# Kernel optimization log

Measured on AMD Instinct MI355X. Metric: run time of the kernel, lower is better.

The kernel has to match this reference:

```python
import jax, jax.numpy as jnp
import numpy as np

N_NODES, N_EDGES = 50000, 800000
IN_CH, HID, HEADS, OUT_CH = 128, 64, 4, 2
NEG_SLOPE = 0.2
EPS = 1e-16


def setup_inputs() -> dict:
    key = jax.random.key(0)
    ks = jax.random.split(key, 16)
    def rn(k, shape, scale=0.1):
        return jax.random.normal(k, shape, dtype=jnp.float32) * scale
    inp = {
        "x": jax.random.normal(ks[0], (N_NODES, IN_CH), dtype=jnp.float32),
        "edge_index": jax.random.randint(ks[1], (2, N_EDGES), 0, N_NODES, dtype=jnp.int64),
        "stats": jax.random.normal(ks[2], (N_EDGES, 3), dtype=jnp.float32),
        # conv1: GATConv(IN_CH -> HID, heads=HEADS, concat=True)
        "W1": rn(ks[3], (IN_CH, HEADS * HID)),
        "att_src1": rn(ks[4], (HEADS, HID)),
        "att_dst1": rn(ks[5], (HEADS, HID)),
        "b1": rn(ks[6], (HEADS * HID,)),
        # conv2: GATConv(HEADS*HID -> HID, heads=1, concat=False)
        "W2": rn(ks[7], (HEADS * HID, HID)),
        "att_src2": rn(ks[8], (1, HID)),
        "att_dst2": rn(ks[9], (1, HID)),
        "b2": rn(ks[10], (HID,)),
        # edge MLP: Linear(2*HID+3 -> HID) -> ReLU -> Linear(HID -> OUT_CH)
        "mW1": rn(ks[11], (2 * HID + 3, HID)),
        "mb1": rn(ks[12], (HID,)),
        "mW2": rn(ks[13], (HID, OUT_CH)),
        "mb2": rn(ks[14], (OUT_CH,)),
    }
    return inp


def gat_layer(x, src, dst, W, att_s, att_d, n_nodes):
    """PyG GATConv core: per-edge attention, softmax over destination, scatter-add."""
    H, C = att_s.shape
    h = (x @ W).reshape(n_nodes, H, C)                      # [N,H,C]
    a_s = jnp.sum(h * att_s, axis=-1)                        # [N,H]
    a_d = jnp.sum(h * att_d, axis=-1)                        # [N,H]
    e = a_s[src] + a_d[dst]                                  # [E,H]
    e = jnp.where(e > 0, e, NEG_SLOPE * e)                   # leaky_relu
    m = jax.ops.segment_max(e, dst, num_segments=n_nodes)    # [N,H]
    m = jnp.where(jnp.isfinite(m), m, 0.0)
    e = jnp.exp(e - m[dst])
    s = jax.ops.segment_sum(e, dst, num_segments=n_nodes)    # [N,H]
    alpha = e / (s[dst] + EPS)                               # [E,H]
    out = jax.ops.segment_sum(alpha[:, :, None] * h[src], dst, num_segments=n_nodes)
    return out                                               # [N,H,C]


def reference(x, edge_index, stats, W1, att_src1, att_dst1, b1,
              W2, att_src2, att_dst2, b2, mW1, mb1, mW2, mb2):
    n = x.shape[0]
    row, col = edge_index[0], edge_index[1]
    # add self loops (PyG GATConv default)
    loop = jnp.arange(n, dtype=edge_index.dtype)
    src = jnp.concatenate([row, loop])
    dst = jnp.concatenate([col, loop])

    # conv1: heads concatenated, then ELU (dropout disabled at inference)
    h1 = gat_layer(x, src, dst, W1, att_src1, att_dst1, n)
    h1 = h1.reshape(n, HEADS * HID) + b1
    h1 = jax.nn.elu(h1)

    # conv2: single head, concat=False (mean over 1 head == squeeze)
    h2 = gat_layer(h1, src, dst, W2, att_src2, att_dst2, n)
    node_emb = h2[:, 0, :] + b2                              # [N,HID]

    # edge MLP over gathered endpoint embeddings + per-edge stats
    feat = jnp.concatenate([node_emb[row], node_emb[col], stats], axis=1)  # [E,2*HID+3]
    hidden = jax.nn.relu(feat @ mW1 + mb1)
    return hidden @ mW2 + mb2                                # [E,OUT_CH]
```

## Files before the change

kernel.cpp:

```cpp
#include <hip/hip_runtime.h>
#include <math.h>

#define NN 50000
#define NE 800000
#define EP (NE + NN)
#define INC 128
#define HID 64
#define HEADS 4
#define C1 (HEADS * HID)
#define NEG 0.2f
#define EPSS 1e-16f

#define SCHUNK 512
#define NSB ((NN + SCHUNK - 1) / SCHUNK)

#define KP1 136
#define KP2 264
typedef __attribute__((ext_vector_type(8))) short bf16x8;
typedef __attribute__((ext_vector_type(4))) float f32x4;

__device__ __forceinline__ unsigned short f2bf(float f) {
    unsigned u = __float_as_uint(f);
    unsigned r = (u + 0x7FFFu + ((u >> 16) & 1u)) >> 16;
    return (unsigned short)r;
}
__device__ __forceinline__ float bf2f(unsigned short b) {
    return __uint_as_float(((unsigned)b) << 16);
}

__global__ __launch_bounds__(SCHUNK) void scan_partial(const int* __restrict__ counts,
                                                       int* __restrict__ bsum) {
    __shared__ int lds[SCHUNK];
    int i = blockIdx.x * SCHUNK + threadIdx.x;
    lds[threadIdx.x] = (i < NN) ? counts[i] : 0;
    __syncthreads();
    for (int off = SCHUNK / 2; off > 0; off >>= 1) {
        if (threadIdx.x < off) lds[threadIdx.x] += lds[threadIdx.x + off];
        __syncthreads();
    }
    if (threadIdx.x == 0) bsum[blockIdx.x] = lds[0];
}

__global__ void scan_top(int* __restrict__ bsum, int* __restrict__ rowptr) {
    __shared__ int lds[NSB];
    int t = threadIdx.x;
    if (t < NSB) lds[t] = bsum[t];
    __syncthreads();
    if (t == 0) {
        int acc = 0;
        for (int i = 0; i < NSB; ++i) { int v = lds[i]; lds[i] = acc; acc += v; }
        rowptr[NN] = acc;
    }
    __syncthreads();
    if (t < NSB) bsum[t] = lds[t];
}

__global__ __launch_bounds__(SCHUNK) void scan_final(const int* __restrict__ counts,
                                                     const int* __restrict__ bsum,
                                                     int* __restrict__ rowptr,
                                                     int* __restrict__ cursor) {
    __shared__ int lds[SCHUNK];
    int i = blockIdx.x * SCHUNK + threadIdx.x;
    int v = (i < NN) ? counts[i] : 0;
    lds[threadIdx.x] = v;
    __syncthreads();
    for (int off = 1; off < SCHUNK; off <<= 1) {
        int t = (threadIdx.x >= off) ? lds[threadIdx.x - off] : 0;
        __syncthreads();
        lds[threadIdx.x] += t;
        __syncthreads();
    }
    if (i < NN) {
        int excl = lds[threadIdx.x] - v + bsum[blockIdx.x];
        rowptr[i] = excl;
        cursor[i] = excl;
    }
}

__global__ void csr_fill(const int* __restrict__ ei, int* __restrict__ cursor,
                         int* __restrict__ csr_src, int* __restrict__ csr_dst) {
    int e = blockIdx.x * 256 + threadIdx.x;
    if (e >= EP) return;
    int s, d;
    if (e < NE) { s = ei[e]; d = ei[NE + e]; } else { s = d = e - NE; }
    int pos = atomicAdd(&cursor[d], 1);
    csr_src[pos] = s;
    csr_dst[pos] = d;
}

#define PREP_N0 (C1 * INC)
#define PREP_N1 (HID * C1)
#define PREP_N2 (5 * 4 * 64 * 8)
#define PREP_TOT (PREP_N0 + PREP_N1 + PREP_N2)
__global__ void prep_all(const float* __restrict__ mW1, const float* __restrict__ W1,
                         const float* __restrict__ W2, const int* __restrict__ ei,
                         unsigned short* __restrict__ w1h, unsigned short* __restrict__ w1l,
                         unsigned short* __restrict__ w2h, unsigned short* __restrict__ w2l,
                         unsigned short* __restrict__ wFh, unsigned short* __restrict__ wFl,
                         int* __restrict__ counts) {
    int i = blockIdx.x * 256 + threadIdx.x;
    if (i < PREP_N0) {
        int c = i >> 7, k = i & 127;
        float f = W1[k * C1 + c];
        unsigned short h = f2bf(f);
        w1h[i] = h; w1l[i] = f2bf(f - bf2f(h));
        return;
    }
    i -= PREP_N0;
    if (i < PREP_N1) {
        int c = i >> 8, k = i & 255;
        float f = W2[k * HID + c];
        unsigned short h = f2bf(f);
        w2h[i] = h; w2l[i] = f2bf(f - bf2f(h));
        return;
    }
    i -= PREP_N1;
    if (i < PREP_N2) {
        int kk = i >> 11;
        int ct = (i >> 9) & 3;
        int l  = (i >> 3) & 63;
        int j  = i & 7;
        int cl = l & 15, g = l >> 4;
        int k   = kk * 32 + g * 8 + j;
        int col = ct * 16 + cl;
        unsigned short h = 0, lo = 0;
        if (k < 131) {
            float f = mW1[k * 64 + col];
            h  = f2bf(f);
            lo = f2bf(f - bf2f(h));
        }
        wFh[i] = h;
        wFl[i] = lo;
        return;
    }
    i -= PREP_N2;
    if (i < EP) {
        int d = (i < NE) ? ei[NE + i] : (i - NE);
        atomicAdd(&counts[d], 1);
    }
}

__global__ void edge_w1k(const int* __restrict__ csr_src, const int* __restrict__ csr_dst,
                         const float* __restrict__ as1, const float* __restrict__ ad1,
                         float* __restrict__ w1e) {
    int i = blockIdx.x * 256 + threadIdx.x;
    if (i >= EP) return;
    int s = csr_src[i], d = csr_dst[i];
    float4 a = *(const float4*)(as1 + s * 4);
    float4 b = *(const float4*)(ad1 + d * 4);
    float4 o;
    float t;
    t = a.x + b.x; t = t > 0.f ? t : NEG * t; o.x = __expf(t);
    t = a.y + b.y; t = t > 0.f ? t : NEG * t; o.y = __expf(t);
    t = a.z + b.z; t = t > 0.f ? t : NEG * t; o.z = __expf(t);
    t = a.w + b.w; t = t > 0.f ? t : NEG * t; o.w = __expf(t);
    *(float4*)(w1e + (size_t)i * 4) = o;
}

__global__ void edge_w2k(const int* __restrict__ csr_src, const int* __restrict__ csr_dst,
                         const float* __restrict__ as2, const float* __restrict__ ad2,
                         float* __restrict__ w2e) {
    int i = blockIdx.x * 256 + threadIdx.x;
    if (i >= EP) return;
    float t = as2[csr_src[i]] + ad2[csr_dst[i]];
    t = t > 0.f ? t : NEG * t;
    w2e[i] = __expf(t);
}

__global__ __launch_bounds__(256) void gemm1_mfma(const float* __restrict__ x,
                                                  const unsigned short* __restrict__ w1h,
                                                  const unsigned short* __restrict__ w1l,
                                                  const float* __restrict__ att_s,
                                                  const float* __restrict__ att_d,
                                                  unsigned short* __restrict__ h1b,
                                                  float* __restrict__ as1,
                                                  float* __restrict__ ad1) {
    __shared__ unsigned short wH[64 * KP1];
    __shared__ unsigned short wL[64 * KP1];
    const int tid = threadIdx.x;
    const int n0 = blockIdx.x * 64;
    const int q  = blockIdx.y;

    for (int idx = tid; idx < 64 * 16; idx += 256) {
        int col = idx >> 4, ch = idx & 15;
        *(bf16x8*)(wH + col * KP1 + ch * 8) =
            *(const bf16x8*)(w1h + ((q * 64 + col) << 7) + ch * 8);
        *(bf16x8*)(wL + col * KP1 + ch * 8) =
            *(const bf16x8*)(w1l + ((q * 64 + col) << 7) + ch * 8);
    }

    const int w = tid >> 6, l = tid & 63;
    const int cl = l & 15, g = l >> 4, g8 = g * 8;
    const int na = min(n0 + w * 16 + cl, NN - 1);

    bf16x8 aH[4], aL[4];
#pragma unroll
    for (int kk = 0; kk < 4; ++kk) {
        const float* ap = x + (size_t)na * INC + kk * 32 + g8;
        float4 v0 = *(const float4*)ap;
        float4 v1 = *(const float4*)(ap + 4);
        float vv[8] = {v0.x, v0.y, v0.z, v0.w, v1.x, v1.y, v1.z, v1.w};
#pragma unroll
        for (int j = 0; j < 8; ++j) {
            unsigned short h = f2bf(vv[j]);
            aH[kk][j] = (short)h;
            aL[kk][j] = (short)f2bf(vv[j] - bf2f(h));
        }
    }

    f32x4 acc[4];
#pragma unroll
    for (int ct = 0; ct < 4; ++ct) acc[ct] = (f32x4){0.f, 0.f, 0.f, 0.f};

    __syncthreads();

#pragma unroll
    for (int kk = 0; kk < 4; ++kk) {
        const int ko = kk * 32 + g8;
#pragma unroll
        for (int ct = 0; ct < 4; ++ct) {
            const bf16x8 bH = *(const bf16x8*)(wH + (ct * 16 + cl) * KP1 + ko);
            const bf16x8 bL = *(const bf16x8*)(wL + (ct * 16 + cl) * KP1 + ko);
            acc[ct] = __builtin_amdgcn_mfma_f32_16x16x32_bf16(aH[kk], bH, acc[ct], 0, 0, 0);
            acc[ct] = __builtin_amdgcn_mfma_f32_16x16x32_bf16(aH[kk], bL, acc[ct], 0, 0, 0);
            acc[ct] = __builtin_amdgcn_mfma_f32_16x16x32_bf16(aL[kk], bH, acc[ct], 0, 0, 0);
        }
    }

    float asc[4], adc[4];
#pragma unroll
    for (int ct = 0; ct < 4; ++ct) {
        asc[ct] = att_s[q * 64 + ct * 16 + cl];
        adc[ct] = att_d[q * 64 + ct * 16 + cl];
    }

#pragma unroll
    for (int reg = 0; reg < 4; ++reg) {
        const int nd = n0 + w * 16 + g * 4 + reg;
        float sa = 0.f, sd = 0.f;
#pragma unroll
        for (int ct = 0; ct < 4; ++ct) {
            sa += acc[ct][reg] * asc[ct];
            sd += acc[ct][reg] * adc[ct];
        }
#pragma unroll
        for (int off = 8; off > 0; off >>= 1) {
            sa += __shfl_xor(sa, off);
            sd += __shfl_xor(sd, off);
        }
        if (nd < NN) {
#pragma unroll
            for (int ct = 0; ct < 4; ++ct)
                h1b[(size_t)nd * C1 + q * 64 + ct * 16 + cl] = f2bf(acc[ct][reg]);
            if (cl == 0) { as1[nd * 4 + q] = sa; ad1[nd * 4 + q] = sd; }
        }
    }
}

__global__ __launch_bounds__(256) void gemm2_mfma(const unsigned short* __restrict__ h1c,
                                                  const unsigned short* __restrict__ w2h,
                                                  const unsigned short* __restrict__ w2l,
                                                  const float* __restrict__ att_s,
                                                  const float* __restrict__ att_d,
                                                  unsigned short* __restrict__ h2b,
                                                  float* __restrict__ as2,
                                                  float* __restrict__ ad2) {
    __shared__ unsigned short wH[64 * KP2];
    __shared__ unsigned short wL[64 * KP2];
    const int tid = threadIdx.x;
    const int n0 = blockIdx.x * 64;

    for (int idx = tid; idx < 64 * 32; idx += 256) {
        int col = idx >> 5, ch = idx & 31;
        *(bf16x8*)(wH + col * KP2 + ch * 8) =
            *(const bf16x8*)(w2h + ((col) << 8) + ch * 8);
        *(bf16x8*)(wL + col * KP2 + ch * 8) =
            *(const bf16x8*)(w2l + ((col) << 8) + ch * 8);
    }

    const int w = tid >> 6, l = tid & 63;
    const int cl = l & 15, g = l >> 4, g8 = g * 8;
    const int na = min(n0 + w * 16 + cl, NN - 1);

    f32x4 acc[4];
#pragma unroll
    for (int ct = 0; ct < 4; ++ct) acc[ct] = (f32x4){0.f, 0.f, 0.f, 0.f};

    __syncthreads();

#pragma unroll
    for (int kk = 0; kk < 8; ++kk) {
        const bf16x8 aH = *(const bf16x8*)(h1c + (size_t)na * C1 + kk * 32 + g8);
        const int ko = kk * 32 + g8;
#pragma unroll
        for (int ct = 0; ct < 4; ++ct) {
            const bf16x8 bH = *(const bf16x8*)(wH + (ct * 16 + cl) * KP2 + ko);
            const bf16x8 bL = *(const bf16x8*)(wL + (ct * 16 + cl) * KP2 + ko);
            acc[ct] = __builtin_amdgcn_mfma_f32_16x16x32_bf16(aH, bH, acc[ct], 0, 0, 0);
            acc[ct] = __builtin_amdgcn_mfma_f32_16x16x32_bf16(aH, bL, acc[ct], 0, 0, 0);
        }
    }

    float asc[4], adc[4];
#pragma unroll
    for (int ct = 0; ct < 4; ++ct) {
        asc[ct] = att_s[ct * 16 + cl];
        adc[ct] = att_d[ct * 16 + cl];
    }

#pragma unroll
    for (int reg = 0; reg < 4; ++reg) {
        const int nd = n0 + w * 16 + g * 4 + reg;
        float sa = 0.f, sd = 0.f;
#pragma unroll
        for (int ct = 0; ct < 4; ++ct) {
            sa += acc[ct][reg] * asc[ct];
            sd += acc[ct][reg] * adc[ct];
        }
#pragma unroll
        for (int off = 8; off > 0; off >>= 1) {
            sa += __shfl_xor(sa, off);
            sd += __shfl_xor(sd, off);
        }
        if (nd < NN) {
#pragma unroll
            for (int ct = 0; ct < 4; ++ct)
                h2b[(size_t)nd * HID + ct * 16 + cl] = f2bf(acc[ct][reg]);
            if (cl == 0) { as2[nd] = sa; ad2[nd] = sd; }
        }
    }
}

__global__ __launch_bounds__(256) void conv1_agg(const int* __restrict__ rowptr,
                                                 const int* __restrict__ csr_src,
                                                 const float* __restrict__ w1e,
                                                 const unsigned short* __restrict__ h1b,
                                                 const float* __restrict__ b1,
                                                 unsigned short* __restrict__ h1c) {
    const int tid  = threadIdx.x;
    const int wid  = tid >> 6;
    const int l    = tid & 63;
    const int half = l >> 5;
    const int l32  = l & 31;
    const int node = blockIdx.x * 8 + wid * 2 + half;
    const int hd   = l32 >> 3;
    const int beg = rowptr[node], end = rowptr[node + 1];

    float acc[8] = {0.f, 0.f, 0.f, 0.f, 0.f, 0.f, 0.f, 0.f};
    float sm = 0.f;
#pragma unroll 2
    for (int i = beg; i < end; ++i) {
        int s = csr_src[i];
        float w = w1e[(size_t)i * 4 + hd];
        bf16x8 hv = *(const bf16x8*)(h1b + (size_t)s * C1 + l32 * 8);
#pragma unroll
        for (int j = 0; j < 8; ++j)
            acc[j] += w * bf2f((unsigned short)hv[j]);
        sm += w;
    }
    const float rden = 1.f / (sm + EPSS);

    const float* bp = b1 + l32 * 8;
    bf16x8 ob;
#pragma unroll
    for (int j = 0; j < 8; ++j) {
        float o = acc[j] * rden + bp[j];
        o = o > 0.f ? o : (__expf(o) - 1.f);
        ob[j] = (short)f2bf(o);
    }
    *(bf16x8*)(h1c + (size_t)node * C1 + l32 * 8) = ob;
}

__global__ __launch_bounds__(256) void conv2_agg(const int* __restrict__ rowptr,
                                                 const int* __restrict__ csr_src,
                                                 const float* __restrict__ w2e,
                                                 const unsigned short* __restrict__ h2b,
                                                 const float* __restrict__ b2,
                                                 unsigned short* __restrict__ embb) {
    const int tid  = threadIdx.x;
    const int wid  = tid >> 6;
    const int l    = tid & 63;
    const int half = l >> 5;
    const int l32  = l & 31;
    const int node = blockIdx.x * 8 + wid * 2 + half;
    const int beg = rowptr[node], end = rowptr[node + 1];

    float a0 = 0.f, a1 = 0.f, sm = 0.f;
#pragma unroll 2
    for (int i = beg; i < end; ++i) {
        int s = csr_src[i];
        float w = w2e[i];
        unsigned hv = *(const unsigned*)(h2b + (size_t)s * HID + l32 * 2);
        a0 += w * bf2f((unsigned short)(hv & 0xFFFF));
        a1 += w * bf2f((unsigned short)(hv >> 16));
        sm += w;
    }
    const float rden = 1.f / (sm + EPSS);
    float o0 = a0 * rden + b2[l32 * 2];
    float o1 = a1 * rden + b2[l32 * 2 + 1];
    unsigned outw = (unsigned)f2bf(o0) | ((unsigned)f2bf(o1) << 16);
    *(unsigned*)(embb + (size_t)node * HID + l32 * 2) = outw;
}

__global__ __launch_bounds__(256) void edge_mlp_mfma(const int* __restrict__ ei,
                                                     const unsigned short* __restrict__ embb,
                                                     const float* __restrict__ stats,
                                                     const unsigned short* __restrict__ wFh,
                                                     const unsigned short* __restrict__ wFl,
                                                     const float* __restrict__ mb1,
                                                     const float* __restrict__ mW2,
                                                     const float* __restrict__ mb2,
                                                     float* __restrict__ out) {
    __shared__ unsigned short sH[PREP_N2];
    __shared__ unsigned short sL[PREP_N2];
    __shared__ float biaS[64], w2aS[64], w2bS[64];
    const int tid = threadIdx.x;
    for (int idx = tid; idx < PREP_N2 / 8; idx += 256) {
        ((float4*)sH)[idx] = ((const float4*)wFh)[idx];
        ((float4*)sL)[idx] = ((const float4*)wFl)[idx];
    }
    if (tid < 64) {
        biaS[tid] = mb1[tid];
        w2aS[tid] = mW2[tid * 2];
        w2bS[tid] = mW2[tid * 2 + 1];
    }

    const int l  = tid & 63;
    const int cl = l & 15;
    const int g  = l >> 4;
    const int g8 = g * 8;
    const float ob0 = mb2[0], ob1 = mb2[1];

    const int t = blockIdx.x * 4 + (tid >> 6);

    bf16x8 a[2][5];
#pragma unroll
    for (int s = 0; s < 2; ++s) {
        const int ge_a = t * 32 + s * 16 + cl;
        const int rn = ei[ge_a];
        const int cn = ei[NE + ge_a];
        const unsigned short* rp = embb + (size_t)rn * HID;
        const unsigned short* cp = embb + (size_t)cn * HID;
        a[s][0] = *(const bf16x8*)(rp + g8);
        a[s][1] = *(const bf16x8*)(rp + 32 + g8);
        a[s][2] = *(const bf16x8*)(cp + g8);
        a[s][3] = *(const bf16x8*)(cp + 32 + g8);
        bf16x8 z = {0, 0, 0, 0, 0, 0, 0, 0};
        if (g == 0) {
            const float* sp = stats + (size_t)ge_a * 3;
            z[0] = (short)f2bf(sp[0]);
            z[1] = (short)f2bf(sp[1]);
            z[2] = (short)f2bf(sp[2]);
        }
        a[s][4] = z;
    }

    f32x4 acc[2][4];
#pragma unroll
    for (int s = 0; s < 2; ++s)
#pragma unroll
        for (int ct = 0; ct < 4; ++ct)
            acc[s][ct] = (f32x4){0.f, 0.f, 0.f, 0.f};

    __syncthreads();

#pragma unroll
    for (int kk = 0; kk < 5; ++kk) {
#pragma unroll
        for (int ct = 0; ct < 4; ++ct) {
            const int fo = ((kk * 4 + ct) * 64 + l) * 8;
            const bf16x8 wHf = *(const bf16x8*)(sH + fo);
            const bf16x8 wLf = *(const bf16x8*)(sL + fo);
#pragma unroll
            for (int s = 0; s < 2; ++s) {
                acc[s][ct] = __builtin_amdgcn_mfma_f32_16x16x32_bf16(wHf, a[s][kk], acc[s][ct], 0, 0, 0);
                acc[s][ct] = __builtin_amdgcn_mfma_f32_16x16x32_bf16(wLf, a[s][kk], acc[s][ct], 0, 0, 0);
            }
        }
    }

#pragma unroll
    for (int s = 0; s < 2; ++s) {
        float p0 = 0.f, p1 = 0.f;
#pragma unroll
        for (int ct = 0; ct < 4; ++ct) {
            const int hb = ct * 16 + g * 4;
            float4 bi = *(const float4*)(biaS + hb);
            float4 wa = *(const float4*)(w2aS + hb);
            float4 wb = *(const float4*)(w2bS + hb);
#pragma unroll
            for (int reg = 0; reg < 4; ++reg) {
                float bv = (reg == 0) ? bi.x : (reg == 1) ? bi.y : (reg == 2) ? bi.z : bi.w;
                float av = (reg == 0) ? wa.x : (reg == 1) ? wa.y : (reg == 2) ? wa.z : wa.w;
                float wv = (reg == 0) ? wb.x : (reg == 1) ? wb.y : (reg == 2) ? wb.z : wb.w;
                float h = fmaxf(acc[s][ct][reg] + bv, 0.f);
                p0 += h * av;
                p1 += h * wv;
            }
        }
        p0 += __shfl_xor(p0, 16); p0 += __shfl_xor(p0, 32);
        p1 += __shfl_xor(p1, 16); p1 += __shfl_xor(p1, 32);
        if (g == 0) {
            const int ge = t * 32 + s * 16 + cl;
            *(float2*)(out + (size_t)ge * 2) = make_float2(p0 + ob0, p1 + ob1);
        }
    }
}

extern "C" void kernel_launch(void* const* d_in, const int* in_sizes, int n_in,
                              void* d_out, int out_size, void* d_ws, size_t ws_size,
                              hipStream_t stream) {
    const float* x      = (const float*)d_in[0];
    const int*   ei     = (const int*)d_in[1];
    const float* stats  = (const float*)d_in[2];
    const float* W1     = (const float*)d_in[3];
    const float* att_s1 = (const float*)d_in[4];
    const float* att_d1 = (const float*)d_in[5];
    const float* b1     = (const float*)d_in[6];
    const float* W2     = (const float*)d_in[7];
    const float* att_s2 = (const float*)d_in[8];
    const float* att_d2 = (const float*)d_in[9];
    const float* b2     = (const float*)d_in[10];
    const float* mW1    = (const float*)d_in[11];
    const float* mb1    = (const float*)d_in[12];
    const float* mW2    = (const float*)d_in[13];
    const float* mb2    = (const float*)d_in[14];
    float* out = (float*)d_out;
    float* ws  = (float*)d_ws;

    int*   rowptr  = (int*)ws;
    int*   csr_src = rowptr + NN + 16;
    int*   csr_dst = csr_src + EP;
    float* as1     = (float*)(csr_dst + EP);
    float* ad1     = as1 + (size_t)4 * NN;
    unsigned short* h1b = (unsigned short*)(ad1 + (size_t)4 * NN);
    unsigned short* h1c = h1b + (size_t)256 * NN;
    unsigned short* h2b = h1c + (size_t)256 * NN;
    unsigned short* embb = h2b + (size_t)64 * NN;
    float* as2     = (float*)(embb + (size_t)64 * NN);
    float* ad2     = as2 + NN;
    unsigned short* w1h = (unsigned short*)(ad2 + NN);
    unsigned short* w1l = w1h + C1 * INC;
    unsigned short* w2h = w1l + C1 * INC;
    unsigned short* w2l = w2h + HID * C1;
    unsigned short* wFh = w2l + HID * C1;
    unsigned short* wFl = wFh + PREP_N2;
    float* w1e     = (float*)(wFl + PREP_N2 + 64);
    float* w2e     = w1e + (size_t)4 * EP;
    int*   counts  = (int*)(w2e + EP + 64);
    int*   bsum    = counts + NN + 64;
    int*   cursor  = bsum + NSB + 64;

    hipMemsetAsync(counts, 0, NN * sizeof(int), stream);
    prep_all<<<(PREP_TOT + EP + 255) / 256, 256, 0, stream>>>(
        mW1, W1, W2, ei, w1h, w1l, w2h, w2l, wFh, wFl, counts);
    scan_partial<<<NSB, SCHUNK, 0, stream>>>(counts, bsum);
    scan_top<<<1, 128, 0, stream>>>(bsum, rowptr);
    scan_final<<<NSB, SCHUNK, 0, stream>>>(counts, bsum, rowptr, cursor);
    csr_fill<<<(EP + 255) / 256, 256, 0, stream>>>(ei, cursor, csr_src, csr_dst);

    gemm1_mfma<<<dim3((NN + 63) / 64, 4), 256, 0, stream>>>(x, w1h, w1l, att_s1, att_d1,
                                                            h1b, as1, ad1);
    edge_w1k<<<(EP + 255) / 256, 256, 0, stream>>>(csr_src, csr_dst, as1, ad1, w1e);
    conv1_agg<<<NN / 8, 256, 0, stream>>>(rowptr, csr_src, w1e, h1b, b1, h1c);

    gemm2_mfma<<<(NN + 63) / 64, 256, 0, stream>>>(h1c, w2h, w2l, att_s2, att_d2,
                                                   h2b, as2, ad2);
    edge_w2k<<<(EP + 255) / 256, 256, 0, stream>>>(csr_src, csr_dst, as2, ad2, w2e);
    conv2_agg<<<NN / 8, 256, 0, stream>>>(rowptr, csr_src, w2e, h2b, b2, embb);

    edge_mlp_mfma<<<(NE / 32) / 4, 256, 0, stream>>>(ei, embb, stats, wFh, wFl,
                                                     mb1, mW2, mb2, out);
}
```

Baseline: 307.9 us.

## Aggregate raw input features before conv1 GEMM and fold attention vectors into W1

Reorders conv1 as aggregate-then-transform: attention logits come from x dotted with precomputed W1·att vectors, per-head weighted sums of bf16 x (128 wide) are gathered per node, and a GEMM with bias and ELU fused follows. This replaces gathering the 256-wide h1 rows per edge with gathering 128-wide x rows, and drops the low-part A MFMA term. The cost is a 4x-wide intermediate (512 per node), lower precision on the aggregated activations, and an extra conversion pass over x in prep. The edge MLP launch is also changed to 512-thread blocks.

New measurement: 308.7 us. No clear change (+0.2%).

```diff
diff --git a/kernel.cpp b/kernel.cpp
--- a/kernel.cpp
+++ b/kernel.cpp
@@ -91,12 +91,17 @@
 #define PREP_N0 (C1 * INC)
 #define PREP_N1 (HID * C1)
 #define PREP_N2 (5 * 4 * 64 * 8)
-#define PREP_TOT (PREP_N0 + PREP_N1 + PREP_N2)
+#define PREP_N3 1024
+#define PREP_N4 (NN * INC)
+#define PREP_TOT (PREP_N0 + PREP_N1 + PREP_N2 + PREP_N3 + PREP_N4)
 __global__ void prep_all(const float* __restrict__ mW1, const float* __restrict__ W1,
                          const float* __restrict__ W2, const int* __restrict__ ei,
+                         const float* __restrict__ x,
+                         const float* __restrict__ att_s1, const float* __restrict__ att_d1,
                          unsigned short* __restrict__ w1h, unsigned short* __restrict__ w1l,
                          unsigned short* __restrict__ w2h, unsigned short* __restrict__ w2l,
                          unsigned short* __restrict__ wFh, unsigned short* __restrict__ wFl,
+                         float* __restrict__ vsd, unsigned short* __restrict__ xb,
                          int* __restrict__ counts) {
     int i = blockIdx.x * 256 + threadIdx.x;
     if (i < PREP_N0) {
@@ -134,9 +139,61 @@
         return;
     }
     i -= PREP_N2;
+    if (i < PREP_N3) {
+        int type = i >> 9;
+        int rem  = i & 511;
+        int h = rem >> 7, k = rem & 127;
+        const float* att = type ? att_d1 : att_s1;
+        float acc = 0.f;
+        for (int c = 0; c < 64; ++c)
+            acc += W1[k * C1 + h * 64 + c] * att[h * 64 + c];
+        vsd[i] = acc;
+        return;
+    }
+    i -= PREP_N3;
+    if (i < PREP_N4) {
+        xb[i] = f2bf(x[i]);
+        return;
+    }
+    i -= PREP_N4;
     if (i < EP) {
         int d = (i < NE) ? ei[NE + i] : (i - NE);
         atomicAdd(&counts[d], 1);
+    }
+}
+
+__global__ __launch_bounds__(256) void att1_kernel(const float* __restrict__ x,
+                                                   const float* __restrict__ vsd,
+                                                   float* __restrict__ as1,
+                                                   float* __restrict__ ad1) {
+    __shared__ float vsS[1024];
+    const int tid = threadIdx.x;
+    for (int idx = tid; idx < 1024; idx += 256) vsS[idx] = vsd[idx];
+    __syncthreads();
+
+    const int n = blockIdx.x * 16 + (tid >> 4);
+    const int l16 = tid & 15;
+    const float* xp = x + (size_t)n * INC + l16 * 8;
+    float4 xa = *(const float4*)xp;
+    float4 xc = *(const float4*)(xp + 4);
+
+    float o[8];
+#pragma unroll
+    for (int h = 0; h < 4; ++h) {
+        const float* vp = vsS + h * 128 + l16 * 8;
+        const float* dp = vsS + 512 + h * 128 + l16 * 8;
+        o[h]     = xa.x * vp[0] + xa.y * vp[1] + xa.z * vp[2] + xa.w * vp[3]
+                 + xc.x * vp[4] + xc.y * vp[5] + xc.z * vp[6] + xc.w * vp[7];
+        o[4 + h] = xa.x * dp[0] + xa.y * dp[1] + xa.z * dp[2] + xa.w * dp[3]
+                 + xc.x * dp[4] + xc.y * dp[5] + xc.z * dp[6] + xc.w * dp[7];
+    }
+#pragma unroll
+    for (int off = 1; off < 16; off <<= 1)
+#pragma unroll
+        for (int v = 0; v < 8; ++v) o[v] += __shfl_xor(o[v], off);
+    if (l16 == 0) {
+        *(float4*)(as1 + n * 4) = make_float4(o[0], o[1], o[2], o[3]);
+        *(float4*)(ad1 + n * 4) = make_float4(o[4], o[5], o[6], o[7]);
     }
 }
 
@@ -167,14 +224,56 @@
     w2e[i] = __expf(t);
 }
 
-__global__ __launch_bounds__(256) void gemm1_mfma(const float* __restrict__ x,
-                                                  const unsigned short* __restrict__ w1h,
-                                                  const unsigned short* __restrict__ w1l,
-                                                  const float* __restrict__ att_s,
-                                                  const float* __restrict__ att_d,
-                                                  unsigned short* __restrict__ h1b,
-                                                  float* __restrict__ as1,
-                                                  float* __restrict__ ad1) {
+__global__ __launch_bounds__(256) void conv1_agg(const int* __restrict__ rowptr,
+                                                 const int* __restrict__ csr_src,
+                                                 const float* __restrict__ w1e,
+                                                 const unsigned short* __restrict__ xb,
+                                                 unsigned short* __restrict__ xaggb) {
+    const int tid = threadIdx.x;
+    const int node = blockIdx.x * 16 + (tid >> 4);
+    const int l16 = tid & 15;
+    const int beg = rowptr[node], end = rowptr[node + 1];
+
+    float acc[4][8];
+#pragma unroll
+    for (int h = 0; h < 4; ++h)
+#pragma unroll
+        for (int j = 0; j < 8; ++j) acc[h][j] = 0.f;
+    float sm[4] = {0.f, 0.f, 0.f, 0.f};
+
+#pragma unroll 2
+    for (int i = beg; i < end; ++i) {
+        int s = csr_src[i];
+        float4 w = *(const float4*)(w1e + (size_t)i * 4);
+        bf16x8 xv = *(const bf16x8*)(xb + (size_t)s * INC + l16 * 8);
+        float xf[8];
+#pragma unroll
+        for (int j = 0; j < 8; ++j) xf[j] = bf2f((unsigned short)xv[j]);
+#pragma unroll
+        for (int j = 0; j < 8; ++j) {
+            acc[0][j] += w.x * xf[j];
+            acc[1][j] += w.y * xf[j];
+            acc[2][j] += w.z * xf[j];
+            acc[3][j] += w.w * xf[j];
+        }
+        sm[0] += w.x; sm[1] += w.y; sm[2] += w.z; sm[3] += w.w;
+    }
+
+#pragma unroll
+    for (int h = 0; h < 4; ++h) {
+        const float rden = 1.f / (sm[h] + EPSS);
+        bf16x8 ob;
+#pragma unroll
+        for (int j = 0; j < 8; ++j) ob[j] = (short)f2bf(acc[h][j] * rden);
+        *(bf16x8*)(xaggb + ((size_t)node * 4 + h) * INC + l16 * 8) = ob;
+    }
+}
+
+__global__ __launch_bounds__(256) void gemm1b(const unsigned short* __restrict__ xaggb,
+                                              const unsigned short* __restrict__ w1h,
+                                              const unsigned short* __restrict__ w1l,
+                                              const float* __restrict__ b1,
+                                              unsigned short* __restrict__ h1c) {
     __shared__ unsigned short wH[64 * KP1];
     __shared__ unsigned short wL[64 * KP1];
     const int tid = threadIdx.x;
@@ -193,20 +292,10 @@
     const int cl = l & 15, g = l >> 4, g8 = g * 8;
     const int na = min(n0 + w * 16 + cl, NN - 1);
 
-    bf16x8 aH[4], aL[4];
-#pragma unroll
-    for (int kk = 0; kk < 4; ++kk) {
-        const float* ap = x + (size_t)na * INC + kk * 32 + g8;
-        float4 v0 = *(const float4*)ap;
-        float4 v1 = *(const float4*)(ap + 4);
-        float vv[8] = {v0.x, v0.y, v0.z, v0.w, v1.x, v1.y, v1.z, v1.w};
-#pragma unroll
-        for (int j = 0; j < 8; ++j) {
-            unsigned short h = f2bf(vv[j]);
-            aH[kk][j] = (short)h;
-            aL[kk][j] = (short)f2bf(vv[j] - bf2f(h));
-        }
-    }
+    bf16x8 aH[4];
+#pragma unroll
+    for (int kk = 0; kk < 4; ++kk)
+        aH[kk] = *(const bf16x8*)(xaggb + ((size_t)na * 4 + q) * INC + kk * 32 + g8);
 
     f32x4 acc[4];
 #pragma unroll
@@ -223,36 +312,20 @@
             const bf16x8 bL = *(const bf16x8*)(wL + (ct * 16 + cl) * KP1 + ko);
             acc[ct] = __builtin_amdgcn_mfma_f32_16x16x32_bf16(aH[kk], bH, acc[ct], 0, 0, 0);
             acc[ct] = __builtin_amdgcn_mfma_f32_16x16x32_bf16(aH[kk], bL, acc[ct], 0, 0, 0);
-            acc[ct] = __builtin_amdgcn_mfma_f32_16x16x32_bf16(aL[kk], bH, acc[ct], 0, 0, 0);
-        }
-    }
-
-    float asc[4], adc[4];
-#pragma unroll
-    for (int ct = 0; ct < 4; ++ct) {
-        asc[ct] = att_s[q * 64 + ct * 16 + cl];
-        adc[ct] = att_d[q * 64 + ct * 16 + cl];
+        }
     }
 
 #pragma unroll
     for (int reg = 0; reg < 4; ++reg) {
         const int nd = n0 + w * 16 + g * 4 + reg;
-        float sa = 0.f, sd = 0.f;
-#pragma unroll
-        for (int ct = 0; ct < 4; ++ct) {
-            sa += acc[ct][reg] * asc[ct];
-            sd += acc[ct][reg] * adc[ct];
-        }
-#pragma unroll
-        for (int off = 8; off > 0; off >>= 1) {
-            sa += __shfl_xor(sa, off);
-            sd += __shfl_xor(sd, off);
-        }
         if (nd < NN) {
 #pragma unroll
-            for (int ct = 0; ct < 4; ++ct)
-                h1b[(size_t)nd * C1 + q * 64 + ct * 16 + cl] = f2bf(acc[ct][reg]);
-            if (cl == 0) { as1[nd * 4 + q] = sa; ad1[nd * 4 + q] = sd; }
+            for (int ct = 0; ct < 4; ++ct) {
+                const int col = q * 64 + ct * 16 + cl;
+                float o = acc[ct][reg] + b1[col];
+                o = o > 0.f ? o : (__expf(o) - 1.f);
+                h1c[(size_t)nd * C1 + col] = f2bf(o);
+            }
         }
     }
 }
@@ -329,46 +402,6 @@
             if (cl == 0) { as2[nd] = sa; ad2[nd] = sd; }
         }
     }
-}
-
-__global__ __launch_bounds__(256) void conv1_agg(const int* __restrict__ rowptr,
-                                                 const int* __restrict__ csr_src,
-                                                 const float* __restrict__ w1e,
-                                                 const unsigned short* __restrict__ h1b,
-                                                 const float* __restrict__ b1,
-                                                 unsigned short* __restrict__ h1c) {
-    const int tid  = threadIdx.x;
-    const int wid  = tid >> 6;
-    const int l    = tid & 63;
-    const int half = l >> 5;
-    const int l32  = l & 31;
-    const int node = blockIdx.x * 8 + wid * 2 + half;
-    const int hd   = l32 >> 3;
-    const int beg = rowptr[node], end = rowptr[node + 1];
-
-    float acc[8] = {0.f, 0.f, 0.f, 0.f, 0.f, 0.f, 0.f, 0.f};
-    float sm = 0.f;
-#pragma unroll 2
-    for (int i = beg; i < end; ++i) {
-        int s = csr_src[i];
-        float w = w1e[(size_t)i * 4 + hd];
-        bf16x8 hv = *(const bf16x8*)(h1b + (size_t)s * C1 + l32 * 8);
-#pragma unroll
-        for (int j = 0; j < 8; ++j)
-            acc[j] += w * bf2f((unsigned short)hv[j]);
-        sm += w;
-    }
-    const float rden = 1.f / (sm + EPSS);
-
-    const float* bp = b1 + l32 * 8;
-    bf16x8 ob;
-#pragma unroll
-    for (int j = 0; j < 8; ++j) {
-        float o = acc[j] * rden + bp[j];
-        o = o > 0.f ? o : (__expf(o) - 1.f);
-        ob[j] = (short)f2bf(o);
-    }
-    *(bf16x8*)(h1c + (size_t)node * C1 + l32 * 8) = ob;
 }
 
 __global__ __launch_bounds__(256) void conv2_agg(const int* __restrict__ rowptr,
@@ -402,7 +435,7 @@
     *(unsigned*)(embb + (size_t)node * HID + l32 * 2) = outw;
 }
 
-__global__ __launch_bounds__(256) void edge_mlp_mfma(const int* __restrict__ ei,
+__global__ __launch_bounds__(512) void edge_mlp_mfma(const int* __restrict__ ei,
                                                      const unsigned short* __restrict__ embb,
                                                      const float* __restrict__ stats,
                                                      const unsigned short* __restrict__ wFh,
@@ -415,7 +448,7 @@
     __shared__ unsigned short sL[PREP_N2];
     __shared__ float biaS[64], w2aS[64], w2bS[64];
     const int tid = threadIdx.x;
-    for (int idx = tid; idx < PREP_N2 / 8; idx += 256) {
+    for (int idx = tid; idx < PREP_N2 / 8; idx += 512) {
         ((float4*)sH)[idx] = ((const float4*)wFh)[idx];
         ((float4*)sL)[idx] = ((const float4*)wFl)[idx];
     }
@@ -431,7 +464,7 @@
     const int g8 = g * 8;
     const float ob0 = mb2[0], ob1 = mb2[1];
 
-    const int t = blockIdx.x * 4 + (tid >> 6);
+    const int t = blockIdx.x * 8 + (tid >> 6);
 
     bf16x8 a[2][5];
 #pragma unroll
@@ -533,10 +566,11 @@
     int*   csr_dst = csr_src + EP;
     float* as1     = (float*)(csr_dst + EP);
     float* ad1     = as1 + (size_t)4 * NN;
-    unsigned short* h1b = (unsigned short*)(ad1 + (size_t)4 * NN);
-    unsigned short* h1c = h1b + (size_t)256 * NN;
-    unsigned short* h2b = h1c + (size_t)256 * NN;
-    unsigned short* embb = h2b + (size_t)64 * NN;
+    unsigned short* xb    = (unsigned short*)(ad1 + (size_t)4 * NN);
+    unsigned short* xaggb = xb + (size_t)128 * NN;
+    unsigned short* h1c   = xaggb + (size_t)512 * NN;
+    unsigned short* h2b   = h1c + (size_t)256 * NN;
+    unsigned short* embb  = h2b + (size_t)64 * NN;
     float* as2     = (float*)(embb + (size_t)64 * NN);
     float* ad2     = as2 + NN;
     unsigned short* w1h = (unsigned short*)(ad2 + NN);
@@ -545,7 +579,8 @@
     unsigned short* w2l = w2h + HID * C1;
     unsigned short* wFh = w2l + HID * C1;
     unsigned short* wFl = wFh + PREP_N2;
-    float* w1e     = (float*)(wFl + PREP_N2 + 64);
+    float* vsd     = (float*)(wFl + PREP_N2);
+    float* w1e     = vsd + 1024;
     float* w2e     = w1e + (size_t)4 * EP;
     int*   counts  = (int*)(w2e + EP + 64);
     int*   bsum    = counts + NN + 64;
@@ -553,22 +588,23 @@
 
     hipMemsetAsync(counts, 0, NN * sizeof(int), stream);
     prep_all<<<(PREP_TOT + EP + 255) / 256, 256, 0, stream>>>(
-        mW1, W1, W2, ei, w1h, w1l, w2h, w2l, wFh, wFl, counts);
+        mW1, W1, W2, ei, x, att_s1, att_d1,
+        w1h, w1l, w2h, w2l, wFh, wFl, vsd, xb, counts);
     scan_partial<<<NSB, SCHUNK, 0, stream>>>(counts, bsum);
     scan_top<<<1, 128, 0, stream>>>(bsum, rowptr);
     scan_final<<<NSB, SCHUNK, 0, stream>>>(counts, bsum, rowptr, cursor);
     csr_fill<<<(EP + 255) / 256, 256, 0, stream>>>(ei, cursor, csr_src, csr_dst);
 
-    gemm1_mfma<<<dim3((NN + 63) / 64, 4), 256, 0, stream>>>(x, w1h, w1l, att_s1, att_d1,
-                                                            h1b, as1, ad1);
+    att1_kernel<<<NN / 16, 256, 0, stream>>>(x, vsd, as1, ad1);
     edge_w1k<<<(EP + 255) / 256, 256, 0, stream>>>(csr_src, csr_dst, as1, ad1, w1e);
-    conv1_agg<<<NN / 8, 256, 0, stream>>>(rowptr, csr_src, w1e, h1b, b1, h1c);
+    conv1_agg<<<NN / 16, 256, 0, stream>>>(rowptr, csr_src, w1e, xb, xaggb);
+    gemm1b<<<dim3((NN + 63) / 64, 4), 256, 0, stream>>>(xaggb, w1h, w1l, b1, h1c);
 
     gemm2_mfma<<<(NN + 63) / 64, 256, 0, stream>>>(h1c, w2h, w2l, att_s2, att_d2,
                                                    h2b, as2, ad2);
     edge_w2k<<<(EP + 255) / 256, 256, 0, stream>>>(csr_src, csr_dst, as2, ad2, w2e);
     conv2_agg<<<NN / 8, 256, 0, stream>>>(rowptr, csr_src, w2e, h2b, b2, embb);
 
-    edge_mlp_mfma<<<(NE / 32) / 4, 256, 0, stream>>>(ei, embb, stats, wFh, wFl,
+    edge_mlp_mfma<<<(NE / 32) / 8, 512, 0, stream>>>(ei, embb, stats, wFh, wFl,
                                                      mb1, mW2, mb2, out);
 }
```
